# Performance work log

Hardware: AMD Instinct MI355X
Metric: run time of the kernel (lower is better)

Reference implementation:

```python
import jax, jax.numpy as jnp
import numpy as np

N = 100000      # nodes
E = 1600000     # edges (avg degree 16)
F_IN = 128      # num_features
H = 64          # hidden_dim
C = 7           # num_classes


def setup_inputs() -> dict:
    key = jax.random.key(0)
    ks = jax.random.split(key, 9)
    x = jax.random.normal(ks[0], (N, F_IN), dtype=jnp.float32)
    edge_index = jax.random.randint(ks[1], (2, E), 0, N, dtype=jnp.int32)
    s1 = 1.0 / np.sqrt(F_IN)
    s2 = 1.0 / np.sqrt(H)
    # SAGEConv1: lin_l applied to aggregated neighbors, lin_r to root
    W1l = jax.random.uniform(ks[2], (F_IN, H), jnp.float32, -s1, s1)
    W1r = jax.random.uniform(ks[3], (F_IN, H), jnp.float32, -s1, s1)
    b1 = jax.random.uniform(ks[4], (H,), jnp.float32, -s1, s1)
    # SAGEConv2
    W2l = jax.random.uniform(ks[5], (H, C), jnp.float32, -s2, s2)
    W2r = jax.random.uniform(ks[6], (H, C), jnp.float32, -s2, s2)
    b2 = jax.random.uniform(ks[7], (C,), jnp.float32, -s2, s2)
    return {"x": x, "edge_index": edge_index, "W1l": W1l, "W1r": W1r,
            "b1": b1, "W2l": W2l, "W2r": W2r, "b2": b2}


def _segment_mean(vals, idx, num_segments):
    # scatter-mean: sum messages per destination node, divide by in-degree
    sums = jax.ops.segment_sum(vals, idx, num_segments=num_segments)
    cnt = jax.ops.segment_sum(jnp.ones(idx.shape, vals.dtype), idx,
                              num_segments=num_segments)
    return sums / jnp.maximum(cnt, 1.0)[:, None]


def reference(x, edge_index, W1l, W1r, b1, W2l, W2r, b2):
    src, dst = edge_index[0], edge_index[1]
    # SAGEConv 1: mean of neighbor (src) features at each dst, plus root term
    agg1 = _segment_mean(x[src], dst, N)              # [N, F_IN]
    h = agg1 @ W1l + x @ W1r + b1                     # [N, H]
    h = jax.nn.relu(h)
    # dropout is inactive in eval mode (deterministic reference)
    # SAGEConv 2
    agg2 = _segment_mean(h[src], dst, N)              # [N, H]
    out = agg2 @ W2l + h @ W2r + b2                   # [N, C]
    return jax.nn.log_softmax(out, axis=1)
```

## Files before the change

### kernel.cpp

```cpp
#include <hip/hip_runtime.h>
#include <cstdint>
#include <cstddef>


#define CAP 64
#define BINSZ 128
#define CH 4096

typedef __attribute__((ext_vector_type(8))) short bf16x8v;
typedef __attribute__((ext_vector_type(4))) float f32x4v;

__device__ __forceinline__ float bf2f(unsigned short u) {
  return __uint_as_float(((unsigned int)u) << 16);
}
__device__ __forceinline__ unsigned short f2bf(float f) {
  unsigned int x = __float_as_uint(f);
  unsigned int r = (x + 0x7fffu + ((x >> 16) & 1u)) >> 16;
  return (unsigned short)r;
}

__global__ __launch_bounds__(256) void k_hist(const int* __restrict__ ei,
                                              int* __restrict__ hist,
                                              const float* __restrict__ W1l,
                                              const float* __restrict__ W1r,
                                              unsigned short* __restrict__ wswz,
                                              int E, int NB, int NCH) {
  const int t = threadIdx.x;
  if (blockIdx.x >= (unsigned)NCH) {
    int idx = (blockIdx.x - NCH) * 256 + t;
    int j = idx & 7;
    int lane = (idx >> 3) & 63;
    int c = (idx >> 9) & 7;
    int t4 = idx >> 12;
    int kk = t4 * 32 + (lane >> 4) * 8 + j;
    int nn = c * 16 + (lane & 15);
    float v = (nn < 64) ? W1l[kk * 64 + nn] : W1r[kk * 64 + (nn - 64)];
    wswz[idx] = f2bf(v);
    return;
  }
  __shared__ int lcnt[1024];
  const int c = blockIdx.x;
  for (int i = t; i < NB; i += 256) lcnt[i] = 0;
  __syncthreads();
  const int base = c * CH;
  const int end = min(base + CH, E);
  for (int e = base + t; e < end; e += 256) {
    int d = ei[E + e];
    atomicAdd(&lcnt[d >> 7], 1);
  }
  __syncthreads();
  for (int i = t; i < NB; i += 256) hist[(size_t)i * NCH + c] = lcnt[i];
}

__global__ __launch_bounds__(256) void k_scanA(int* __restrict__ hist,
                                               int* __restrict__ tot,
                                               int NB, int NCH) {
  const int lane = threadIdx.x & 63;
  const int bin = blockIdx.x * 4 + (threadIdx.x >> 6);
  if (bin >= NB) return;
  int* h = hist + (size_t)bin * NCH;
  int carry = 0;
  for (int base = 0; base < NCH; base += 64) {
    int i = base + lane;
    int v = (i < NCH) ? h[i] : 0;
    int incl = v;
    #pragma unroll
    for (int d = 1; d < 64; d <<= 1) {
      int t = __shfl_up(incl, d, 64);
      if (lane >= d) incl += t;
    }
    if (i < NCH) h[i] = carry + incl - v;
    carry += __shfl(incl, 63, 64);
  }
  if (lane == 0) tot[bin] = carry;
}

__global__ __launch_bounds__(64) void k_scanB(const int* __restrict__ tot,
                                              int* __restrict__ binbase, int NB) {
  const int lane = threadIdx.x;
  int carry = 0;
  for (int base = 0; base < NB; base += 64) {
    int i = base + lane;
    int v = (i < NB) ? tot[i] : 0;
    int incl = v;
    #pragma unroll
    for (int d = 1; d < 64; d <<= 1) {
      int t = __shfl_up(incl, d, 64);
      if (lane >= d) incl += t;
    }
    if (i < NB) binbase[i] = carry + incl - v;
    carry += __shfl(incl, 63, 64);
  }
  if (lane == 0) binbase[NB] = carry;
}

__global__ __launch_bounds__(256) void k_scat(const int* __restrict__ ei,
                                              const int* __restrict__ hist,
                                              const int* __restrict__ binbase,
                                              unsigned int* __restrict__ part,
                                              int E, int NB, int NCH) {
  __shared__ int lcur[1024];
  const int c = blockIdx.x, t = threadIdx.x;
  for (int i = t; i < NB; i += 256)
    lcur[i] = hist[(size_t)i * NCH + c] + binbase[i];
  __syncthreads();
  const int base = c * CH;
  const int end = min(base + CH, E);
  for (int e = base + t; e < end; e += 256) {
    int s = ei[e];
    int d = ei[E + e];
    int bin = d >> 7;
    int pos = atomicAdd(&lcur[bin], 1);
    part[pos] = (unsigned)s | ((unsigned)(d & 127) << 17);
  }
}

__global__ __launch_bounds__(256) void k_bucketB(const int* __restrict__ binbase,
                                                 const unsigned int* __restrict__ part,
                                                 int* __restrict__ cnt,
                                                 int* __restrict__ bucket) {
  __shared__ int lbkt[BINSZ * CAP];
  __shared__ int ldeg[BINSZ];
  const int b = blockIdx.x, t = threadIdx.x;
  if (t < BINSZ) ldeg[t] = 0;
  __syncthreads();
  const int e0 = binbase[b], e1 = binbase[b + 1];
  for (int i = e0 + t; i < e1; i += 256) {
    unsigned rec = part[i];
    int loc = rec >> 17;
    int p = atomicAdd(&ldeg[loc], 1);
    if (p < CAP) lbkt[loc * CAP + p] = (int)(rec & 0x1FFFFu);
  }
  __syncthreads();
  if (t < BINSZ) cnt[b * BINSZ + t] = ldeg[t];
  const int4* s4 = (const int4*)lbkt;
  int4* d4 = (int4*)(bucket + (size_t)b * BINSZ * CAP);
  #pragma unroll 2
  for (int i = t; i < BINSZ * CAP / 4; i += 256) d4[i] = s4[i];
}

__global__ __launch_bounds__(256) void k_gemm1(
    const float* __restrict__ x,
    const unsigned short* __restrict__ wswz,
    const float* __restrict__ b1,
    unsigned short* __restrict__ xl,
    unsigned short* __restrict__ hroot,
    int Nn) {
  __shared__ unsigned short Bsw[16384];
  const int t = threadIdx.x;
  {
    const uint4* src = (const uint4*)wswz;
    uint4* dst = (uint4*)Bsw;
    #pragma unroll
    for (int i = 0; i < 8; ++i) dst[t + i * 256] = src[t + i * 256];
  }
  __syncthreads();

  const int lane = t & 63;
  const int wid = t >> 6;
  const int quad = lane >> 4;
  const int m = lane & 15;
  const int rowA = blockIdx.x * 64 + wid * 16 + m;
  const float* xrow = x + (size_t)min(rowA, Nn - 1) * 128;

  f32x4v acc[8];
  #pragma unroll
  for (int c = 0; c < 8; ++c) acc[c] = (f32x4v){0.f, 0.f, 0.f, 0.f};

  #pragma unroll
  for (int t4 = 0; t4 < 4; ++t4) {
    const int koff = t4 * 32 + quad * 8;
    float4 a0 = *(const float4*)(xrow + koff);
    float4 a1 = *(const float4*)(xrow + koff + 4);
    bf16x8v af;
    af[0] = (short)f2bf(a0.x); af[1] = (short)f2bf(a0.y);
    af[2] = (short)f2bf(a0.z); af[3] = (short)f2bf(a0.w);
    af[4] = (short)f2bf(a1.x); af[5] = (short)f2bf(a1.y);
    af[6] = (short)f2bf(a1.z); af[7] = (short)f2bf(a1.w);
    #pragma unroll
    for (int c = 0; c < 8; ++c) {
      const bf16x8v bf_ = *(const bf16x8v*)&Bsw[(((t4 * 8 + c) * 64 + lane)) << 3];
      acc[c] = __builtin_amdgcn_mfma_f32_16x16x32_bf16(af, bf_, acc[c], 0, 0, 0);
    }
  }

  const int rbase = blockIdx.x * 64 + wid * 16 + quad * 4;
  #pragma unroll
  for (int c = 0; c < 8; ++c) {
    const int col = c * 16 + m;
    #pragma unroll
    for (int i = 0; i < 4; ++i) {
      const int r = rbase + i;
      if (r < Nn) {
        if (c < 4) xl[(size_t)r * 64 + col] = f2bf(acc[c][i]);
        else       hroot[(size_t)r * 64 + (col - 64)] = f2bf(acc[c][i] + b1[col - 64]);
      }
    }
  }
}

__global__ __launch_bounds__(256) void k_agg1(
    const int* __restrict__ cnt, const int* __restrict__ bucket,
    const unsigned int* __restrict__ xl32, const unsigned int* __restrict__ hroot32,
    unsigned int* __restrict__ hbuf32, int Nn) {
  const int lane = threadIdx.x & 63;
  const int q = lane & 15;
  const int g = lane >> 4;
  const int gw = blockIdx.x * (blockDim.x >> 6) + (threadIdx.x >> 6);
  const int nw = gridDim.x * (blockDim.x >> 6);
  for (int n = gw; n < Nn; n += nw) {
    int c = cnt[n];
    int m = c < CAP ? c : CAP;
    int sidx = (lane < m) ? bucket[(size_t)n * CAP + lane] : 0;
    if ((unsigned)sidx >= (unsigned)Nn) sidx = 0;
    uint2 hu = *(const uint2*)(hroot32 + (size_t)n * 32 + 2 * q);
    float a0 = 0.f, a1 = 0.f, a2 = 0.f, a3 = 0.f;
    int i = 0;
    for (; i + 16 <= m; i += 16) {
      int rA = __shfl(sidx, i + g, 64);
      int rB = __shfl(sidx, i + 4 + g, 64);
      int rC = __shfl(sidx, i + 8 + g, 64);
      int rD = __shfl(sidx, i + 12 + g, 64);
      uint2 uA = *(const uint2*)(xl32 + (size_t)rA * 32 + 2 * q);
      uint2 uB = *(const uint2*)(xl32 + (size_t)rB * 32 + 2 * q);
      uint2 uC = *(const uint2*)(xl32 + (size_t)rC * 32 + 2 * q);
      uint2 uD = *(const uint2*)(xl32 + (size_t)rD * 32 + 2 * q);
      a0 += (__uint_as_float(uA.x << 16) + __uint_as_float(uB.x << 16))
          + (__uint_as_float(uC.x << 16) + __uint_as_float(uD.x << 16));
      a1 += (__uint_as_float(uA.x & 0xFFFF0000u) + __uint_as_float(uB.x & 0xFFFF0000u))
          + (__uint_as_float(uC.x & 0xFFFF0000u) + __uint_as_float(uD.x & 0xFFFF0000u));
      a2 += (__uint_as_float(uA.y << 16) + __uint_as_float(uB.y << 16))
          + (__uint_as_float(uC.y << 16) + __uint_as_float(uD.y << 16));
      a3 += (__uint_as_float(uA.y & 0xFFFF0000u) + __uint_as_float(uB.y & 0xFFFF0000u))
          + (__uint_as_float(uC.y & 0xFFFF0000u) + __uint_as_float(uD.y & 0xFFFF0000u));
    }
    for (; i + 8 <= m; i += 8) {
      int rA = __shfl(sidx, i + g, 64);
      int rB = __shfl(sidx, i + 4 + g, 64);
      uint2 uA = *(const uint2*)(xl32 + (size_t)rA * 32 + 2 * q);
      uint2 uB = *(const uint2*)(xl32 + (size_t)rB * 32 + 2 * q);
      a0 += __uint_as_float(uA.x << 16) + __uint_as_float(uB.x << 16);
      a1 += __uint_as_float(uA.x & 0xFFFF0000u) + __uint_as_float(uB.x & 0xFFFF0000u);
      a2 += __uint_as_float(uA.y << 16) + __uint_as_float(uB.y << 16);
      a3 += __uint_as_float(uA.y & 0xFFFF0000u) + __uint_as_float(uB.y & 0xFFFF0000u);
    }
    for (; i < m; i += 4) {
      int e = i + g;
      int r = __shfl(sidx, e & 63, 64);
      uint2 u = *(const uint2*)(xl32 + (size_t)r * 32 + 2 * q);
      if (e < m) {
        a0 += __uint_as_float(u.x << 16);
        a1 += __uint_as_float(u.x & 0xFFFF0000u);
        a2 += __uint_as_float(u.y << 16);
        a3 += __uint_as_float(u.y & 0xFFFF0000u);
      }
    }
    a0 += __shfl_xor(a0, 16, 64); a0 += __shfl_xor(a0, 32, 64);
    a1 += __shfl_xor(a1, 16, 64); a1 += __shfl_xor(a1, 32, 64);
    a2 += __shfl_xor(a2, 16, 64); a2 += __shfl_xor(a2, 32, 64);
    a3 += __shfl_xor(a3, 16, 64); a3 += __shfl_xor(a3, 32, 64);
    if (g == 0) {
      float dd = c > 0 ? (float)c : 1.f;
      float h0 = fmaxf(a0 / dd + __uint_as_float(hu.x << 16), 0.f);
      float h1 = fmaxf(a1 / dd + __uint_as_float(hu.x & 0xFFFF0000u), 0.f);
      float h2 = fmaxf(a2 / dd + __uint_as_float(hu.y << 16), 0.f);
      float h3 = fmaxf(a3 / dd + __uint_as_float(hu.y & 0xFFFF0000u), 0.f);
      uint2 o;
      o.x = (unsigned)f2bf(h0) | ((unsigned)f2bf(h1) << 16);
      o.y = (unsigned)f2bf(h2) | ((unsigned)f2bf(h3) << 16);
      *(uint2*)(hbuf32 + (size_t)n * 32 + 2 * q) = o;
    }
  }
}

__global__ __launch_bounds__(128) void k_gemm2(
    const unsigned short* __restrict__ hbuf,
    const float* __restrict__ W2l, const float* __restrict__ W2r,
    const float* __restrict__ b2,
    float* __restrict__ hl, float* __restrict__ hr, int Nn) {
  __shared__ float tile[128 * 65];
  const int t = threadIdx.x;
  const int rowbase = blockIdx.x * 128;
  for (int idx = t; idx < 128 * 64; idx += 128) {
    int r = idx >> 6, k = idx & 63;
    int n = rowbase + r;
    tile[r * 65 + k] = (n < Nn) ? bf2f(hbuf[(size_t)n * 64 + k]) : 0.f;
  }
  __syncthreads();
  int n = rowbase + t;
  if (n >= Nn) return;
  float al[7] = {0, 0, 0, 0, 0, 0, 0};
  float ar[7] = {0, 0, 0, 0, 0, 0, 0};
  for (int k = 0; k < 64; ++k) {
    float hv = tile[t * 65 + k];
    #pragma unroll
    for (int c = 0; c < 7; ++c) {
      al[c] = fmaf(hv, W2l[k * 7 + c], al[c]);
      ar[c] = fmaf(hv, W2r[k * 7 + c], ar[c]);
    }
  }
  #pragma unroll
  for (int c = 0; c < 7; ++c) {
    hl[(size_t)n * 8 + c] = al[c];
    hr[(size_t)n * 8 + c] = ar[c] + b2[c];
  }
  hl[(size_t)n * 8 + 7] = 0.f;
  hr[(size_t)n * 8 + 7] = 0.f;
}

__global__ __launch_bounds__(256) void k_out(
    const int* __restrict__ cnt, const int* __restrict__ bucket,
    const float* __restrict__ hl, const float* __restrict__ hr,
    float* __restrict__ out, int Nn) {
  const int lane = threadIdx.x & 63;
  const int c = lane & 7;
  const int sub = lane >> 3;
  const int gw = blockIdx.x * (blockDim.x >> 6) + (threadIdx.x >> 6);
  const int n = gw * 8 + sub;
  if (n >= Nn) return;
  int cn = cnt[n];
  int m = cn < CAP ? cn : CAP;
  const bool act = (c < 7);
  float acc = 0.f;
  for (int e0 = 0; e0 < m; e0 += 8) {
    int bv = (e0 + c < m) ? bucket[(size_t)n * CAP + e0 + c] : 0;
    #pragma unroll
    for (int cc = 0; cc < 8; ++cc) {
      if (e0 + cc < m) {
        int s = __shfl(bv, (lane & 56) + cc, 64);
        if ((unsigned)s >= (unsigned)Nn) s = 0;
        if (act) acc += hl[(size_t)s * 8 + c];
      }
    }
  }
  float dd = cn > 0 ? (float)cn : 1.f;
  float v = act ? (acc / dd + hr[(size_t)n * 8 + c]) : -INFINITY;
  float mx = v;
  mx = fmaxf(mx, __shfl_xor(mx, 1, 8));
  mx = fmaxf(mx, __shfl_xor(mx, 2, 8));
  mx = fmaxf(mx, __shfl_xor(mx, 4, 8));
  float ex = act ? expf(v - mx) : 0.f;
  float s2 = ex;
  s2 += __shfl_xor(s2, 1, 8);
  s2 += __shfl_xor(s2, 2, 8);
  s2 += __shfl_xor(s2, 4, 8);
  float res = v - mx - logf(s2);
  if (act) out[(size_t)n * 7 + c] = res;
}

static inline size_t alignup(size_t v) { return (v + 255) & ~(size_t)255; }

extern "C" void kernel_launch(void* const* d_in, const int* in_sizes, int n_in,
                              void* d_out, int out_size, void* d_ws, size_t ws_size,
                              hipStream_t stream) {
  const int N = in_sizes[0] / 128;
  const int E = in_sizes[1] / 2;
  const int NB = (N + BINSZ - 1) / BINSZ;
  const int Np = NB * BINSZ;
  const int NCH = (E + CH - 1) / CH;

  const float* x   = (const float*)d_in[0];
  const int*   ei  = (const int*)d_in[1];
  const float* W1l = (const float*)d_in[2];
  const float* W1r = (const float*)d_in[3];
  const float* b1  = (const float*)d_in[4];
  const float* W2l = (const float*)d_in[5];
  const float* W2r = (const float*)d_in[6];
  const float* b2  = (const float*)d_in[7];
  float* out = (float*)d_out;

  char* p = (char*)d_ws;
  int* hist    = (int*)p;            p += alignup((size_t)NB * NCH * 4);
  int* tot     = (int*)p;            p += alignup((size_t)NB * 4);
  int* binbase = (int*)p;            p += alignup((size_t)(NB + 1) * 4);
  unsigned int* part = (unsigned int*)p; p += alignup((size_t)E * 4);
  int* cnt    = (int*)p;             p += alignup((size_t)Np * 4);
  int* bucket = (int*)p;             p += alignup((size_t)Np * CAP * 4);
  unsigned short* wswz = (unsigned short*)p; p += alignup((size_t)16384 * 2);
  unsigned short* xl    = (unsigned short*)p; p += alignup((size_t)N * 64 * 2);
  unsigned short* hroot = (unsigned short*)p; p += alignup((size_t)N * 64 * 2);
  unsigned short* hbuf  = (unsigned short*)p; p += alignup((size_t)N * 64 * 2);
  float* hl  = (float*)p;            p += alignup((size_t)N * 8 * 4);
  float* hr  = (float*)p;            p += alignup((size_t)N * 8 * 4);

  dim3 b256(256);
  k_hist<<<dim3(NCH + 64), b256, 0, stream>>>(ei, hist, W1l, W1r, wswz, E, NB, NCH);
  k_scanA<<<dim3((NB + 3) / 4), b256, 0, stream>>>(hist, tot, NB, NCH);
  k_scanB<<<dim3(1), dim3(64), 0, stream>>>(tot, binbase, NB);
  k_scat<<<dim3(NCH), b256, 0, stream>>>(ei, hist, binbase, part, E, NB, NCH);
  k_bucketB<<<dim3(NB), b256, 0, stream>>>(binbase, part, cnt, bucket);
  k_gemm1<<<dim3((N + 63) / 64), b256, 0, stream>>>(x, wswz, b1, xl, hroot, N);
  k_agg1<<<dim3(2048), b256, 0, stream>>>(cnt, bucket,
      (const unsigned int*)xl, (const unsigned int*)hroot, (unsigned int*)hbuf, N);
  k_gemm2<<<dim3((N + 127) / 128), dim3(128), 0, stream>>>(hbuf, W2l, W2r, b2, hl, hr, N);
  const int waves_out = (N + 7) / 8;
  k_out<<<dim3((waves_out + 3) / 4), b256, 0, stream>>>(cnt, bucket, hl, hr, out, N);
}
```

Before: 256.3 us.

## Process two nodes per wavefront in layer-1 aggregation using half-wave split

Splits each 64-lane wavefront into two 32-lane halves, each aggregating a different destination node, with two edges handled per step per half and eight gathers in flight per unrolled iteration. This is meant to cut the idle lanes and shuffle-reduction overhead that come from low-degree nodes (average degree 16) occupying a whole wave. In exchange, loops run to the larger of the two halves' degrees, with per-edge predication, so load imbalance between paired nodes wastes some work.

```diff
diff --git a/kernel.cpp b/kernel.cpp
--- a/kernel.cpp
+++ b/kernel.cpp
@@ -204,62 +204,100 @@
     const unsigned int* __restrict__ xl32, const unsigned int* __restrict__ hroot32,
     unsigned int* __restrict__ hbuf32, int Nn) {
   const int lane = threadIdx.x & 63;
-  const int q = lane & 15;
-  const int g = lane >> 4;
+  const int half = lane >> 5;
+  const int hlane = lane & 31;
+  const int q = hlane & 15;
+  const int g = hlane >> 4;
+  const int sb = lane & 32;
   const int gw = blockIdx.x * (blockDim.x >> 6) + (threadIdx.x >> 6);
   const int nw = gridDim.x * (blockDim.x >> 6);
-  for (int n = gw; n < Nn; n += nw) {
-    int c = cnt[n];
+  for (int n0 = gw * 2; n0 < Nn; n0 += nw * 2) {
+    const int n = n0 + half;
+    const bool vn = (n < Nn);
+    const int nc = vn ? n : (Nn - 1);
+    int c = cnt[nc];
     int m = c < CAP ? c : CAP;
-    int sidx = (lane < m) ? bucket[(size_t)n * CAP + lane] : 0;
-    if ((unsigned)sidx >= (unsigned)Nn) sidx = 0;
-    uint2 hu = *(const uint2*)(hroot32 + (size_t)n * 32 + 2 * q);
+    if (!vn) m = 0;
+    int sA = (hlane < m) ? bucket[(size_t)nc * 64 + hlane] : 0;
+    int sB = (hlane + 32 < m) ? bucket[(size_t)nc * 64 + 32 + hlane] : 0;
+    if ((unsigned)sA >= (unsigned)Nn) sA = 0;
+    if ((unsigned)sB >= (unsigned)Nn) sB = 0;
+    uint2 hu = *(const uint2*)(hroot32 + (size_t)nc * 32 + 2 * q);
+    int mo = __shfl_xor(m, 32, 64);
+    const int mm = m > mo ? m : mo;
     float a0 = 0.f, a1 = 0.f, a2 = 0.f, a3 = 0.f;
+
+#define ACCP(u, e) {                                         \
+    unsigned vx = ((e) < m) ? (u).x : 0u;                    \
+    unsigned vy = ((e) < m) ? (u).y : 0u;                    \
+    a0 += __uint_as_float(vx << 16);                         \
+    a1 += __uint_as_float(vx & 0xFFFF0000u);                 \
+    a2 += __uint_as_float(vy << 16);                         \
+    a3 += __uint_as_float(vy & 0xFFFF0000u); }
+
     int i = 0;
-    for (; i + 16 <= m; i += 16) {
-      int rA = __shfl(sidx, i + g, 64);
-      int rB = __shfl(sidx, i + 4 + g, 64);
-      int rC = __shfl(sidx, i + 8 + g, 64);
-      int rD = __shfl(sidx, i + 12 + g, 64);
-      uint2 uA = *(const uint2*)(xl32 + (size_t)rA * 32 + 2 * q);
-      uint2 uB = *(const uint2*)(xl32 + (size_t)rB * 32 + 2 * q);
-      uint2 uC = *(const uint2*)(xl32 + (size_t)rC * 32 + 2 * q);
-      uint2 uD = *(const uint2*)(xl32 + (size_t)rD * 32 + 2 * q);
-      a0 += (__uint_as_float(uA.x << 16) + __uint_as_float(uB.x << 16))
-          + (__uint_as_float(uC.x << 16) + __uint_as_float(uD.x << 16));
-      a1 += (__uint_as_float(uA.x & 0xFFFF0000u) + __uint_as_float(uB.x & 0xFFFF0000u))
-          + (__uint_as_float(uC.x & 0xFFFF0000u) + __uint_as_float(uD.x & 0xFFFF0000u));
-      a2 += (__uint_as_float(uA.y << 16) + __uint_as_float(uB.y << 16))
-          + (__uint_as_float(uC.y << 16) + __uint_as_float(uD.y << 16));
-      a3 += (__uint_as_float(uA.y & 0xFFFF0000u) + __uint_as_float(uB.y & 0xFFFF0000u))
-          + (__uint_as_float(uC.y & 0xFFFF0000u) + __uint_as_float(uD.y & 0xFFFF0000u));
-    }
-    for (; i + 8 <= m; i += 8) {
-      int rA = __shfl(sidx, i + g, 64);
-      int rB = __shfl(sidx, i + 4 + g, 64);
-      uint2 uA = *(const uint2*)(xl32 + (size_t)rA * 32 + 2 * q);
-      uint2 uB = *(const uint2*)(xl32 + (size_t)rB * 32 + 2 * q);
-      a0 += __uint_as_float(uA.x << 16) + __uint_as_float(uB.x << 16);
-      a1 += __uint_as_float(uA.x & 0xFFFF0000u) + __uint_as_float(uB.x & 0xFFFF0000u);
-      a2 += __uint_as_float(uA.y << 16) + __uint_as_float(uB.y << 16);
-      a3 += __uint_as_float(uA.y & 0xFFFF0000u) + __uint_as_float(uB.y & 0xFFFF0000u);
-    }
-    for (; i < m; i += 4) {
-      int e = i + g;
-      int r = __shfl(sidx, e & 63, 64);
-      uint2 u = *(const uint2*)(xl32 + (size_t)r * 32 + 2 * q);
-      if (e < m) {
-        a0 += __uint_as_float(u.x << 16);
-        a1 += __uint_as_float(u.x & 0xFFFF0000u);
-        a2 += __uint_as_float(u.y << 16);
-        a3 += __uint_as_float(u.y & 0xFFFF0000u);
-      }
-    }
-    a0 += __shfl_xor(a0, 16, 64); a0 += __shfl_xor(a0, 32, 64);
-    a1 += __shfl_xor(a1, 16, 64); a1 += __shfl_xor(a1, 32, 64);
-    a2 += __shfl_xor(a2, 16, 64); a2 += __shfl_xor(a2, 32, 64);
-    a3 += __shfl_xor(a3, 16, 64); a3 += __shfl_xor(a3, 32, 64);
-    if (g == 0) {
+    for (; i + 16 <= mm; i += 16) {
+      int src = (i < 32) ? sA : sB;
+      int eb = i & 32;
+      int r0 = __shfl(src, sb + (i      + g - eb), 64);
+      int r1 = __shfl(src, sb + (i + 2  + g - eb), 64);
+      int r2 = __shfl(src, sb + (i + 4  + g - eb), 64);
+      int r3 = __shfl(src, sb + (i + 6  + g - eb), 64);
+      int r4 = __shfl(src, sb + (i + 8  + g - eb), 64);
+      int r5 = __shfl(src, sb + (i + 10 + g - eb), 64);
+      int r6 = __shfl(src, sb + (i + 12 + g - eb), 64);
+      int r7 = __shfl(src, sb + (i + 14 + g - eb), 64);
+      uint2 u0 = *(const uint2*)(xl32 + (size_t)r0 * 32 + 2 * q);
+      uint2 u1 = *(const uint2*)(xl32 + (size_t)r1 * 32 + 2 * q);
+      uint2 u2 = *(const uint2*)(xl32 + (size_t)r2 * 32 + 2 * q);
+      uint2 u3 = *(const uint2*)(xl32 + (size_t)r3 * 32 + 2 * q);
+      uint2 u4 = *(const uint2*)(xl32 + (size_t)r4 * 32 + 2 * q);
+      uint2 u5 = *(const uint2*)(xl32 + (size_t)r5 * 32 + 2 * q);
+      uint2 u6 = *(const uint2*)(xl32 + (size_t)r6 * 32 + 2 * q);
+      uint2 u7 = *(const uint2*)(xl32 + (size_t)r7 * 32 + 2 * q);
+      ACCP(u0, i + g);      ACCP(u1, i + 2 + g);
+      ACCP(u2, i + 4 + g);  ACCP(u3, i + 6 + g);
+      ACCP(u4, i + 8 + g);  ACCP(u5, i + 10 + g);
+      ACCP(u6, i + 12 + g); ACCP(u7, i + 14 + g);
+    }
+    if (i + 8 <= mm) {
+      int src = (i < 32) ? sA : sB;
+      int eb = i & 32;
+      int r0 = __shfl(src, sb + (i     + g - eb), 64);
+      int r1 = __shfl(src, sb + (i + 2 + g - eb), 64);
+      int r2 = __shfl(src, sb + (i + 4 + g - eb), 64);
+      int r3 = __shfl(src, sb + (i + 6 + g - eb), 64);
+      uint2 u0 = *(const uint2*)(xl32 + (size_t)r0 * 32 + 2 * q);
+      uint2 u1 = *(const uint2*)(xl32 + (size_t)r1 * 32 + 2 * q);
+      uint2 u2 = *(const uint2*)(xl32 + (size_t)r2 * 32 + 2 * q);
+      uint2 u3 = *(const uint2*)(xl32 + (size_t)r3 * 32 + 2 * q);
+      ACCP(u0, i + g);     ACCP(u1, i + 2 + g);
+      ACCP(u2, i + 4 + g); ACCP(u3, i + 6 + g);
+      i += 8;
+    }
+    if (i + 4 <= mm) {
+      int src = (i < 32) ? sA : sB;
+      int eb = i & 32;
+      int r0 = __shfl(src, sb + (i     + g - eb), 64);
+      int r1 = __shfl(src, sb + (i + 2 + g - eb), 64);
+      uint2 u0 = *(const uint2*)(xl32 + (size_t)r0 * 32 + 2 * q);
+      uint2 u1 = *(const uint2*)(xl32 + (size_t)r1 * 32 + 2 * q);
+      ACCP(u0, i + g); ACCP(u1, i + 2 + g);
+      i += 4;
+    }
+    for (; i < mm; i += 2) {
+      int src = (i < 32) ? sA : sB;
+      int eb = i & 32;
+      int r0 = __shfl(src, sb + (i + g - eb), 64);
+      uint2 u0 = *(const uint2*)(xl32 + (size_t)r0 * 32 + 2 * q);
+      ACCP(u0, i + g);
+    }
+#undef ACCP
+    a0 += __shfl_xor(a0, 16, 64);
+    a1 += __shfl_xor(a1, 16, 64);
+    a2 += __shfl_xor(a2, 16, 64);
+    a3 += __shfl_xor(a3, 16, 64);
+    if (vn && g == 0) {
       float dd = c > 0 ? (float)c : 1.f;
       float h0 = fmaxf(a0 / dd + __uint_as_float(hu.x << 16), 0.f);
       float h1 = fmaxf(a1 / dd + __uint_as_float(hu.x & 0xFFFF0000u), 0.f);
```

Result: no change. 254.2 us (-0.8%).
